# Performance work log

Hardware: AMD Instinct MI355X
Metric: run time of the kernel (lower is better)

## Reference

```python
import jax, jax.numpy as jnp
import numpy as np

GROUPS = 8   # GroupNorm groups used by create_pat_conv*_blocks(..., groups=8)
EPS = 1e-5
K = 20       # num_neighbor


def group_norm(x, gamma, beta):
    # x: [B, C, ...spatial]
    B, C = x.shape[0], x.shape[1]
    shape = x.shape
    xg = x.reshape(B, GROUPS, C // GROUPS, -1)
    m = xg.mean(axis=(2, 3), keepdims=True)
    v = ((xg - m) ** 2).mean(axis=(2, 3), keepdims=True)
    xg = (xg - m) * jax.lax.rsqrt(v + EPS)
    x = xg.reshape(shape)
    bshape = (1, C) + (1,) * (len(shape) - 2)
    return x * gamma.reshape(bshape) + beta.reshape(bshape)


def conv_block(x, w, b, gamma, beta):
    # pointwise (kernel-size 1) conv + GroupNorm + ELU, works for 1d and 2d spatial
    y = jnp.einsum('oc,bc...->bo...', w, x) + b.reshape((1, -1) + (1,) * (x.ndim - 2))
    return jax.nn.elu(group_norm(y, gamma, beta))


def knn_graph(points, k):
    # points: [B, 3, N] -> neighbor coords [B, 3, N, k] (self included, dilation=1)
    sq = jnp.sum(points * points, axis=1)                      # [B, N]
    inner = jnp.einsum('bci,bcj->bij', points, points)         # [B, N, N]
    dist = sq[:, :, None] + sq[:, None, :] - 2.0 * inner       # squared pairwise dist
    _, idx = jax.lax.top_k(-dist, k)                           # [B, N, k] smallest dists
    neighbors = jnp.take_along_axis(points[:, :, None, :], idx[:, None, :, :], axis=3)
    return neighbors                                           # [B, 3, N, k]


def setup_inputs() -> dict:
    key = jax.random.key(0)
    B, N = 4, 8192
    dims1 = [6, 32, 64]
    dims2 = [64, 512, 1024]
    keys = iter(jax.random.split(key, 32))
    inp = {"points": jax.random.normal(next(keys), (B, 3, N), dtype=jnp.float32)}
    for tag, dims in (("p1", dims1), ("p2", dims2)):
        for i in range(len(dims) - 1):
            cin, cout = dims[i], dims[i + 1]
            inp[f"{tag}_w{i}"] = jax.random.normal(next(keys), (cout, cin), dtype=jnp.float32) / np.float32(np.sqrt(cin))
            inp[f"{tag}_b{i}"] = jnp.zeros((cout,), dtype=jnp.float32)
            inp[f"{tag}_g{i}"] = jnp.ones((cout,), dtype=jnp.float32)
            inp[f"{tag}_beta{i}"] = jnp.zeros((cout,), dtype=jnp.float32)
    return inp


def reference(points, p1_w0, p1_b0, p1_g0, p1_beta0, p1_w1, p1_b1, p1_g1, p1_beta1,
              p2_w0, p2_b0, p2_g0, p2_beta0, p2_w1, p2_b1, p2_g1, p2_beta1):
    neighbors = knn_graph(points, K)                             # [B, 3, N, K]
    center = jnp.broadcast_to(points[:, :, :, None], neighbors.shape)
    x = jnp.concatenate([center, neighbors - center], axis=1)   # [B, 6, N, K]
    x = conv_block(x, p1_w0, p1_b0, p1_g0, p1_beta0)            # [B, 32, N, K]
    x = conv_block(x, p1_w1, p1_b1, p1_g1, p1_beta1)            # [B, 64, N, K]
    x = jnp.max(x, axis=2)                                      # [B, 64, K] (faithful to source: max over dim=2)
    x = conv_block(x, p2_w0, p2_b0, p2_g0, p2_beta0)            # [B, 512, K]
    x = conv_block(x, p2_w1, p2_b1, p2_g1, p2_beta1)            # [B, 1024, K]
    return x
```

## Files before the change

kernel.cpp:

```cpp
#include <hip/hip_runtime.h>
#include <math.h>

#define NPTS   8192
#define BATCH  4
#define KNN    20
#define NKTOT  (NPTS*KNN)
#define EPS    1e-5f
#define QC2    16
#define FQC    64

#define WINW   3072
#define WITR   (WINW/4/128)
#define NBIN   1024
#define BIN_LO (-4.5f)
#define BIN_W  (9.0f/1024.0f)

typedef float v2f __attribute__((ext_vector_type(2)));

__device__ __forceinline__ float elu(float x) { return x > 0.0f ? x : expm1f(x); }
__device__ __forceinline__ float eluf(float x) { return x > 0.0f ? x : __expf(x) - 1.0f; }
__device__ __forceinline__ v2f splat2(float x) { v2f v; v.x = x; v.y = x; return v; }
__device__ __forceinline__ float rfl(float x) {
    return __uint_as_float(__builtin_amdgcn_readfirstlane(__float_as_uint(x)));
}

__device__ __forceinline__ unsigned fenc(float f) {
    unsigned b = __float_as_uint(f);
    return b ^ ((unsigned)(((int)b) >> 31) | 0x80000000u);
}
__device__ __forceinline__ float fdec(unsigned u) {
    unsigned b = (u & 0x80000000u) ? (u ^ 0x80000000u) : ~u;
    return __uint_as_float(b);
}

__device__ __forceinline__ int xbin(float x) {
    int bin = (int)floorf((x + 4.5f) * (1024.0f / 9.0f));
    return bin < 0 ? 0 : (bin > NBIN - 1 ? NBIN - 1 : bin);
}

__device__ __forceinline__ unsigned long long packkey(float s, int orig, int slot) {
    return ((unsigned long long)fenc(s) << 32)
         | (unsigned)(((NPTS - 1 - orig) << 13) | slot);
}

__global__ __launch_bounds__(256) void prep_kernel(const float* __restrict__ points,
                                                   float4* __restrict__ pts4,
                                                   float* __restrict__ zeroreg,
                                                   unsigned* __restrict__ minenc,
                                                   unsigned* __restrict__ fcnt)
{
    const int t = blockIdx.x * 256 + threadIdx.x;
    const int b = t >> 13, n = t & (NPTS - 1);
    const float* px = points + b * 3 * NPTS;
    float x = px[n], y = px[NPTS + n], z = px[2 * NPTS + n];
    pts4[t] = make_float4(x, y, z, -0.5f * (x * x + y * y + z * z));
    if (t < 18176) zeroreg[t] = 0.f;
    if (t < 5120)  minenc[t] = 0xFFFFFFFFu;
    if (t < 4)     fcnt[t] = 0u;
}

__global__ __launch_bounds__(1024) void hist_kernel(const float* __restrict__ points,
                                                    int* __restrict__ Pcur)
{
    __shared__ int h[NBIN];
    __shared__ int sc[NBIN];
    const int b = blockIdx.x;
    const int t = threadIdx.x;
    h[t] = 0;
    __syncthreads();
    const float* px = points + b * 3 * NPTS;
    for (int i = t; i < NPTS; i += 1024)
        atomicAdd(&h[xbin(px[i])], 1);
    __syncthreads();
    int v = h[t];
    sc[t] = v;
    __syncthreads();
    for (int off = 1; off < NBIN; off <<= 1) {
        int a = (t >= off) ? sc[t - off] : 0;
        __syncthreads();
        sc[t] += a;
        __syncthreads();
    }
    Pcur[b * NBIN + t] = sc[t] - v;
}

__global__ __launch_bounds__(256) void scatter_kernel(const float4* __restrict__ pts4,
                                                      int* __restrict__ Pcur,
                                                      float4* __restrict__ psort,
                                                      int* __restrict__ sidx,
                                                      int* __restrict__ binof)
{
    const int t = blockIdx.x * 256 + threadIdx.x;
    const int b = t >> 13, n = t & (NPTS - 1);
    float4 p = pts4[t];
    int bin = xbin(p.x);
    int slot = atomicAdd(&Pcur[b * NBIN + bin], 1);
    psort[b * NPTS + slot] = p;
    sidx [b * NPTS + slot] = n;
    binof[b * NPTS + slot] = bin;
}

__global__ __launch_bounds__(256, 8) void knn_win_kernel(
    const float4* __restrict__ psort, const int* __restrict__ sidx,
    const int* __restrict__ binof, int* __restrict__ idx_out,
    unsigned* __restrict__ fcnt, int* __restrict__ flist)
{
    __shared__ unsigned long long queue[32][QC2];
    __shared__ float smaxs[4][8][64];
    __shared__ float gates[8];
    __shared__ int qcnt[32];

    const int tid  = threadIdx.x;
    const int lane = tid & 63;
    const int wv   = tid >> 6;
    const int b    = blockIdx.x >> 10;
    const int oct  = blockIdx.x & 1023;
    const int q0s  = oct * 8;
    const float4* psb = psort + b * NPTS;
    const int*    six = sidx  + b * NPTS;
    const int*    bob = binof + b * NPTS;

    int s = q0s + 4 - WINW / 2;
    if (s < 0) s = 0;
    if (s > NPTS - WINW) s = NPTS - WINW;

    if (tid < 32) qcnt[tid] = 0;

    float qx[8], qy[8], qz[8], q2[8];
    v2f smax2[8];
#pragma unroll
    for (int q = 0; q < 8; ++q) {
        float4 qp = psb[q0s + q];
        qx[q] = rfl(qp.x); qy[q] = rfl(qp.y); qz[q] = rfl(qp.z);
        q2[q] = rfl(-(qp.w + qp.w));
        smax2[q] = splat2(-INFINITY);
    }

    const int lbase = s + (((lane >> 5) * 4 + wv) << 6) + ((lane & 31) << 1);

#pragma unroll 3
    for (int t = 0; t < WITR; ++t) {
        float4 p0 = psb[lbase + t * 512];
        float4 p1 = psb[lbase + t * 512 + 1];
        v2f px = { p0.x, p1.x }, py = { p0.y, p1.y };
        v2f pz = { p0.z, p1.z }, pw = { p0.w, p1.w };
#pragma unroll
        for (int q = 0; q < 8; ++q) {
            v2f sv = __builtin_elementwise_fma(splat2(qx[q]), px,
                     __builtin_elementwise_fma(splat2(qy[q]), py,
                     __builtin_elementwise_fma(splat2(qz[q]), pz, pw)));
            smax2[q] = __builtin_elementwise_max(smax2[q], sv);
        }
    }
#pragma unroll
    for (int q = 0; q < 8; ++q) smaxs[wv][q][lane] = fmaxf(smax2[q].x, smax2[q].y);
    __syncthreads();

#pragma unroll
    for (int qq = 0; qq < 2; ++qq) {
        const int q = wv * 2 + qq;
        float v = fmaxf(fmaxf(smaxs[0][q][lane], smaxs[1][q][lane]),
                        fmaxf(smaxs[2][q][lane], smaxs[3][q][lane]));
#pragma unroll
        for (int k = 2; k <= 64; k <<= 1)
#pragma unroll
            for (int j = k >> 1; j >= 1; j >>= 1) {
                float o = __shfl_xor(v, j);
                bool up = ((lane & k) == 0);
                bool keepmin = (((lane & j) == 0) == up);
                v = keepmin ? fminf(v, o) : fmaxf(v, o);
            }
        float m = __shfl(v, 44);
        if (lane == 0) gates[q] = m - 1e-4f - 1e-5f * fabsf(m);
    }
    __syncthreads();
    float sgate[8];
#pragma unroll
    for (int q = 0; q < 8; ++q) sgate[q] = gates[q];

    for (int t = 0; t < WITR; ++t) {
        const int jb = lbase + t * 512;
        float4 p0 = psb[jb];
        float4 p1 = psb[jb + 1];
        v2f px = { p0.x, p1.x }, py = { p0.y, p1.y };
        v2f pz = { p0.z, p1.z }, pw = { p0.w, p1.w };
#pragma unroll
        for (int q = 0; q < 8; ++q) {
            v2f sv = __builtin_elementwise_fma(splat2(qx[q]), px,
                     __builtin_elementwise_fma(splat2(qy[q]), py,
                     __builtin_elementwise_fma(splat2(qz[q]), pz, pw)));
            if (fmaxf(sv.x, sv.y) >= sgate[q]) {
#pragma unroll
                for (int h = 0; h < 2; ++h) {
                    float svh = h ? sv.y : sv.x;
                    if (svh >= sgate[q]) {
                        int slot = atomicAdd(&qcnt[wv * 8 + q], 1);
                        if (slot < QC2)
                            queue[wv * 8 + q][slot] = packkey(svh, six[jb + h], jb + h);
                    }
                }
            }
        }
    }
    __syncthreads();

    float xLe = (s == 0) ? -3.0e38f
                         : (BIN_LO + (float)(bob[s] + 1) * BIN_W);
    float xRe = (s == NPTS - WINW) ? 3.0e38f
                         : (BIN_LO + (float)bob[s + WINW] * BIN_W);

#pragma unroll
    for (int qq = 0; qq < 2; ++qq) {
        const int q = wv * 2 + qq;
        int c0r = qcnt[0 * 8 + q], c1r = qcnt[1 * 8 + q];
        int c2r = qcnt[2 * 8 + q], c3r = qcnt[3 * 8 + q];
        const bool ovf = (c0r > QC2) || (c1r > QC2) || (c2r > QC2) || (c3r > QC2);
        int c0 = c0r < QC2 ? c0r : QC2;
        int c1 = c1r < QC2 ? c1r : QC2;
        int c2 = c2r < QC2 ? c2r : QC2;
        int c3 = c3r < QC2 ? c3r : QC2;
        int b1 = c0, b2 = c0 + c1, b3 = c0 + c1 + c2, b4 = b3 + c3;
        unsigned long long key = 0ull;
        if (lane < b1)      key = queue[0 * 8 + q][lane];
        else if (lane < b2) key = queue[1 * 8 + q][lane - b1];
        else if (lane < b3) key = queue[2 * 8 + q][lane - b2];
        else if (lane < b4) key = queue[3 * 8 + q][lane - b3];
#pragma unroll
        for (int k = 2; k <= 64; k <<= 1)
#pragma unroll
            for (int j = k >> 1; j >= 1; j >>= 1) {
                unsigned long long o = __shfl_xor(key, j);
                bool up = ((lane & k) == 0);
                bool keepmax = (((lane & j) == 0) == up);
                bool omax = o > key;
                key = (keepmax == omax) ? o : key;
            }
        if (lane < KNN)
            idx_out[(b * KNN + lane) * NPTS + (q0s + q)] =
                (int)(unsigned)(key & 0x1FFFu);

        unsigned long long k19 = __shfl(key, 19);
        float s20 = fdec((unsigned)(k19 >> 32));
        float d20 = fmaxf(q2[q] - 2.0f * s20, 0.0f);
        float mg  = 1e-3f + 1e-3f * d20;
        float dL  = qx[q] - xLe;
        float dR  = xRe - qx[q];
        bool ok = !ovf && dL > 0.0f && dR > 0.0f
                  && (d20 + mg < dL * dL) && (d20 + mg < dR * dR);
        if (!ok && lane == 0) {
            unsigned fs = atomicAdd(&fcnt[b], 1u);
            if (fs < 8192u) flist[b * 8192 + fs] = q0s + q;
        }
    }
}

__global__ __launch_bounds__(256, 8) void knn_fb_kernel(const float4* __restrict__ psort,
                                                        const int* __restrict__ sidx,
                                                        int* __restrict__ idx_out,
                                                        const unsigned* __restrict__ fcnt,
                                                        const int* __restrict__ flist)
{
    __shared__ unsigned long long queue[2][FQC];
    __shared__ float smaxs[4][2][64];
    __shared__ float gates[2];
    __shared__ int qcnt[2];

    const int tid  = threadIdx.x;
    const int lane = tid & 63;
    const int wv   = tid >> 6;
    const int bb   = blockIdx.x & 3;
    unsigned cnt = fcnt[bb];
    if (cnt > 8192u) cnt = 8192u;
    if (cnt == 0u) return;
    const float4* pb = psort + bb * NPTS;
    const int* six = sidx + bb * NPTS;
    const int* fl = flist + bb * 8192;
    const int cbase = wv * (NPTS / 4);
    const int tstep = gridDim.x >> 2;

    for (int task = blockIdx.x >> 2; task * 2 < (int)cnt; task += tstep) {
        int qs[2];
        float qx[2], qy[2], qz[2];
        v2f smax2[2];
        if (tid < 2) qcnt[tid] = 0;
#pragma unroll
        for (int q = 0; q < 2; ++q) {
            int e = task * 2 + q;
            if (e >= (int)cnt) e = (int)cnt - 1;
            qs[q] = __builtin_amdgcn_readfirstlane(fl[e]);
            float4 qp = pb[qs[q]];
            qx[q] = rfl(qp.x); qy[q] = rfl(qp.y); qz[q] = rfl(qp.z);
            smax2[q] = splat2(-INFINITY);
        }

#pragma unroll 4
        for (int t = 0; t < NPTS / 4 / 128; ++t) {
            float4 p0 = pb[cbase + t * 128 + 2 * lane];
            float4 p1 = pb[cbase + t * 128 + 2 * lane + 1];
            v2f px = { p0.x, p1.x }, py = { p0.y, p1.y };
            v2f pz = { p0.z, p1.z }, pw = { p0.w, p1.w };
#pragma unroll
            for (int q = 0; q < 2; ++q) {
                v2f sv = __builtin_elementwise_fma(splat2(qx[q]), px,
                         __builtin_elementwise_fma(splat2(qy[q]), py,
                         __builtin_elementwise_fma(splat2(qz[q]), pz, pw)));
                smax2[q] = __builtin_elementwise_max(smax2[q], sv);
            }
        }
#pragma unroll
        for (int q = 0; q < 2; ++q) smaxs[wv][q][lane] = fmaxf(smax2[q].x, smax2[q].y);
        __syncthreads();

        if (wv < 2) {
            const int q = wv;
            float v = fmaxf(fmaxf(smaxs[0][q][lane], smaxs[1][q][lane]),
                            fmaxf(smaxs[2][q][lane], smaxs[3][q][lane]));
#pragma unroll
            for (int k = 2; k <= 64; k <<= 1)
#pragma unroll
                for (int j = k >> 1; j >= 1; j >>= 1) {
                    float o = __shfl_xor(v, j);
                    bool up = ((lane & k) == 0);
                    bool keepmin = (((lane & j) == 0) == up);
                    v = keepmin ? fminf(v, o) : fmaxf(v, o);
                }
            float m = __shfl(v, 44);
            if (lane == 0) gates[q] = m - 1e-4f - 1e-5f * fabsf(m);
        }
        __syncthreads();
        float sg0 = gates[0], sg1 = gates[1];

        for (int t = 0; t < NPTS / 4 / 128; ++t) {
            const int jb = cbase + t * 128 + 2 * lane;
            float4 p0 = pb[jb];
            float4 p1 = pb[jb + 1];
            v2f px = { p0.x, p1.x }, py = { p0.y, p1.y };
            v2f pz = { p0.z, p1.z }, pw = { p0.w, p1.w };
#pragma unroll
            for (int q = 0; q < 2; ++q) {
                float sg = q ? sg1 : sg0;
                v2f sv = __builtin_elementwise_fma(splat2(qx[q]), px,
                         __builtin_elementwise_fma(splat2(qy[q]), py,
                         __builtin_elementwise_fma(splat2(qz[q]), pz, pw)));
                if (fmaxf(sv.x, sv.y) >= sg) {
#pragma unroll
                    for (int h = 0; h < 2; ++h) {
                        float svh = h ? sv.y : sv.x;
                        if (svh >= sg) {
                            int slot = atomicAdd(&qcnt[q], 1);
                            if (slot < FQC)
                                queue[q][slot] = packkey(svh, six[jb + h], jb + h);
                        }
                    }
                }
            }
        }
        __syncthreads();

        if (wv < 2) {
            const int q = wv;
            int c = qcnt[q]; c = c < FQC ? c : FQC;
            unsigned long long key = (lane < c) ? queue[q][lane] : 0ull;
#pragma unroll
            for (int k = 2; k <= 64; k <<= 1)
#pragma unroll
                for (int j = k >> 1; j >= 1; j >>= 1) {
                    unsigned long long o = __shfl_xor(key, j);
                    bool up = ((lane & k) == 0);
                    bool keepmax = (((lane & j) == 0) == up);
                    bool omax = o > key;
                    key = (keepmax == omax) ? o : key;
                }
            if (lane < KNN)
                idx_out[(bb * KNN + lane) * NPTS + qs[q]] =
                    (int)(unsigned)(key & 0x1FFFu);
        }
        __syncthreads();
    }
}

__global__ __launch_bounds__(256) void moments_x_kernel(const float4* __restrict__ psort,
                                                        const int* __restrict__ idx,
                                                        float* __restrict__ sums1p)
{
    const int b  = blockIdx.x / 80;
    const int r0 = (blockIdx.x - b * 80) * 2048;
    const float4* pb = psort + b * NPTS;
    const int* ib = idx + b * NKTOT;

    float v[27];
#pragma unroll
    for (int i = 0; i < 27; ++i) v[i] = 0.f;

    for (int e = 0; e < 8; ++e) {
        const int id = r0 + e * 256 + threadIdx.x;
        const int n = id & (NPTS - 1);
        const int j = ib[id];
        float4 c4 = pb[n];
        float4 e4 = pb[j];
        float x[6] = { c4.x, c4.y, c4.z, e4.x - c4.x, e4.y - c4.y, e4.z - c4.z };
        int p = 6;
#pragma unroll
        for (int d = 0; d < 6; ++d) {
            v[d] += x[d];
#pragma unroll
            for (int ee = d; ee < 6; ++ee) v[p++] += x[d] * x[ee];
        }
    }
#pragma unroll
    for (int i = 0; i < 27; ++i)
        for (int o = 32; o > 0; o >>= 1) v[i] += __shfl_xor(v[i], o);

    __shared__ float red[4][27];
    const int lane = threadIdx.x & 63, w = threadIdx.x >> 6;
    if (lane == 0)
#pragma unroll
        for (int i = 0; i < 27; ++i) red[w][i] = v[i];
    __syncthreads();
    if (threadIdx.x < 27) {
        float acc = red[0][threadIdx.x] + red[1][threadIdx.x] + red[2][threadIdx.x] + red[3][threadIdx.x];
        int slot = blockIdx.x & 63;
        atomicAdd(&sums1p[(slot * BATCH + b) * 27 + threadIdx.x], acc);
    }
}

__global__ void finalize1_kernel(const float* __restrict__ sums1p,
                                 const float* __restrict__ w1, const float* __restrict__ b1,
                                 const float* __restrict__ g1, const float* __restrict__ beta1,
                                 float* __restrict__ w1f)
{
    __shared__ float S[BATCH][27];
    const int t = threadIdx.x;
    if (t < 108) {
        int b = t / 27, i = t % 27;
        float acc = 0.f;
        for (int s = 0; s < 64; ++s) acc += sums1p[(s * BATCH + b) * 27 + i];
        S[b][i] = acc;
    }
    __syncthreads();
    const int b = t >> 5, c = t & 31;
    const float invS = 1.0f / (float)NKTOT;
    float Ex[6], M[6][6];
#pragma unroll
    for (int d = 0; d < 6; ++d) Ex[d] = S[b][d] * invS;
    int p = 6;
#pragma unroll
    for (int d = 0; d < 6; ++d)
#pragma unroll
        for (int e = d; e < 6; ++e) { float v = S[b][p++] * invS; M[d][e] = v; M[e][d] = v; }
    const int g = c >> 2;
    float msum = 0.f, qsum = 0.f;
    for (int cc = g * 4; cc < g * 4 + 4; ++cc) {
        float w[6];
#pragma unroll
        for (int d = 0; d < 6; ++d) w[d] = w1[cc * 6 + d];
        float dotEx = 0.f;
#pragma unroll
        for (int d = 0; d < 6; ++d) dotEx += w[d] * Ex[d];
        float Ey = dotEx + b1[cc];
        float Ey2 = 0.f;
#pragma unroll
        for (int d = 0; d < 6; ++d)
#pragma unroll
            for (int e = 0; e < 6; ++e) Ey2 += w[d] * w[e] * M[d][e];
        Ey2 += 2.0f * b1[cc] * dotEx + b1[cc] * b1[cc];
        msum += Ey; qsum += Ey2;
    }
    float m = msum * 0.25f;
    float var = qsum * 0.25f - m * m;
    float inv = rsqrtf(var + EPS);
    float s = g1[c] * inv;
    float tt = s * (b1[c] - m) + beta1[c];
    float* o = w1f + (b * 32 + c) * 8;
#pragma unroll
    for (int d = 0; d < 6; ++d) o[d] = s * w1[c * 6 + d];
    o[6] = tt; o[7] = 0.f;
}

__global__ __launch_bounds__(256, 3) void fused_main_kernel(
    const float4* __restrict__ psort, const int* __restrict__ idxb,
    const float* __restrict__ w1f, const float* __restrict__ w2, const float* __restrict__ b2,
    float* __restrict__ sums2p, unsigned int* __restrict__ maxenc, unsigned int* __restrict__ minenc)
{
    __shared__ __align__(16) float w2t[32 * 64];
    __shared__ __align__(16) float z1s[32 * 256];
    __shared__ __align__(16) float4 w1s4[64];
    __shared__ float b2s[64];
    __shared__ float redmx[256], redmn[256], sqred[64];

    const int t   = threadIdx.x;
    const int blk = blockIdx.x;
    const int nc  = blk & 15;
    const int k   = (blk >> 4) % 20;
    const int b   = blk / 320;

    for (int i = t; i < 512; i += 256) {
        float4 v = ((const float4*)w2)[i];
        int c = i >> 3, kq = (i & 7) * 4;
        w2t[(kq + 0) * 64 + c] = v.x; w2t[(kq + 1) * 64 + c] = v.y;
        w2t[(kq + 2) * 64 + c] = v.z; w2t[(kq + 3) * 64 + c] = v.w;
    }
    if (t < 64) { w1s4[t] = ((const float4*)w1f)[b * 64 + t]; b2s[t] = b2[t]; }

    const int wvi = t >> 6;
    const int cg8 = t & 7;
    const int n0  = (t >> 3) * 8;
    const int c0  = cg8 * 8;
    const float4* pb = psort + b * NPTS;
    const int nbase = nc * 512;
    const int* idxrow = idxb + (b * KNN + k) * NPTS;

    float mx[8], mn[8];
#pragma unroll
    for (int ci = 0; ci < 8; ++ci) { mx[ci] = -INFINITY; mn[ci] = INFINITY; }
    float gs = 0.f, gq = 0.f;

    for (int ph = 0; ph < 2; ++ph) {
        const int n = nbase + ph * 256 + t;
        const int j = idxrow[n];
        float4 c4 = pb[n];
        float4 e4 = pb[j];
        float x0[6] = { c4.x, c4.y, c4.z, e4.x - c4.x, e4.y - c4.y, e4.z - c4.z };

        __syncthreads();
#pragma unroll
        for (int c = 0; c < 32; ++c) {
            float4 wA = w1s4[c * 2 + 0];
            float4 wB = w1s4[c * 2 + 1];
            float z = wB.z;
            z = fmaf(wA.x, x0[0], z); z = fmaf(wA.y, x0[1], z); z = fmaf(wA.z, x0[2], z);
            z = fmaf(wA.w, x0[3], z); z = fmaf(wB.x, x0[4], z); z = fmaf(wB.y, x0[5], z);
            z1s[c * 256 + t] = eluf(z);
        }
        __syncthreads();

        float acc[8][8];
#pragma unroll
        for (int ci = 0; ci < 8; ++ci) {
            float bb = b2s[c0 + ci];
#pragma unroll
            for (int pj = 0; pj < 8; ++pj) acc[ci][pj] = bb;
        }
#pragma unroll
        for (int kk = 0; kk < 32; ++kk) {
            float4 a0 = *(const float4*)&w2t[kk * 64 + c0];
            float4 a1 = *(const float4*)&w2t[kk * 64 + c0 + 4];
            float4 z0 = *(const float4*)&z1s[kk * 256 + n0];
            float4 z1v = *(const float4*)&z1s[kk * 256 + n0 + 4];
            float avv[8] = { a0.x, a0.y, a0.z, a0.w, a1.x, a1.y, a1.z, a1.w };
            float zvv[8] = { z0.x, z0.y, z0.z, z0.w, z1v.x, z1v.y, z1v.z, z1v.w };
#pragma unroll
            for (int ci = 0; ci < 8; ++ci)
#pragma unroll
                for (int pj = 0; pj < 8; ++pj) acc[ci][pj] = fmaf(avv[ci], zvv[pj], acc[ci][pj]);
        }
#pragma unroll
        for (int ci = 0; ci < 8; ++ci)
#pragma unroll
            for (int pj = 0; pj < 8; ++pj) {
                float v = acc[ci][pj];
                gs += v; gq = fmaf(v, v, gq);
                mx[ci] = fmaxf(mx[ci], v); mn[ci] = fminf(mn[ci], v);
            }
    }

#pragma unroll
    for (int m = 8; m <= 32; m <<= 1) {
#pragma unroll
        for (int ci = 0; ci < 8; ++ci) {
            mx[ci] = fmaxf(mx[ci], __shfl_xor(mx[ci], m));
            mn[ci] = fminf(mn[ci], __shfl_xor(mn[ci], m));
        }
        gs += __shfl_xor(gs, m);
        gq += __shfl_xor(gq, m);
    }
    if ((t & 63) < 8) {
        const int l = t & 7;
#pragma unroll
        for (int ci = 0; ci < 8; ++ci) {
            redmx[wvi * 64 + l * 8 + ci] = mx[ci];
            redmn[wvi * 64 + l * 8 + ci] = mn[ci];
        }
        sqred[(wvi * 8 + l) * 2 + 0] = gs;
        sqred[(wvi * 8 + l) * 2 + 1] = gq;
    }
    __syncthreads();
    if (t < 64) {
        float m = fmaxf(fmaxf(redmx[t], redmx[64 + t]), fmaxf(redmx[128 + t], redmx[192 + t]));
        atomicMax(&maxenc[(b * 64 + t) * KNN + k], fenc(m));
    } else if (t < 128) {
        int c = t - 64;
        float m = fminf(fminf(redmn[c], redmn[64 + c]), fminf(redmn[128 + c], redmn[192 + c]));
        atomicMin(&minenc[(b * 64 + c) * KNN + k], fenc(m));
    } else if (t < 144) {
        int i2 = t - 128, g = i2 >> 1, w = i2 & 1;
        float v = 0.f;
#pragma unroll
        for (int wv2 = 0; wv2 < 4; ++wv2)
            v += sqred[(wv2 * 8 + g) * 2 + w];
        int slot = blk & 63;
        atomicAdd(&sums2p[((slot * BATCH + b) * 8 + g) * 2 + w], v);
    }
}

__global__ void build_m1_kernel(const float* __restrict__ sums2p,
                                const unsigned int* __restrict__ maxenc,
                                const unsigned int* __restrict__ minenc,
                                const float* __restrict__ gamma, const float* __restrict__ beta,
                                float* __restrict__ m1)
{
    const int t = blockIdx.x * 256 + threadIdx.x;
    const int b = t / 1280;
    const int r = t - b * 1280;
    const int c = r / 20;
    const int g = c >> 3;
    float s = 0.f, q = 0.f;
    for (int sl = 0; sl < 64; ++sl) {
        s += sums2p[((sl * BATCH + b) * 8 + g) * 2 + 0];
        q += sums2p[((sl * BATCH + b) * 8 + g) * 2 + 1];
    }
    const float cnt = 8.0f * (float)NKTOT;
    float m = s / cnt;
    float var = q / cnt - m * m;
    float inv = rsqrtf(var + EPS);
    float sc = gamma[c] * inv;
    float tt = beta[c] - sc * m;
    float y = (sc >= 0.f) ? fdec(maxenc[t]) : fdec(minenc[t]);
    m1[t] = elu(sc * y + tt);
}

template <int CIN, int SLOTS>
__global__ void p2_gemm_kernel(const float* __restrict__ zin, const float* __restrict__ w,
                               const float* __restrict__ bias, float* __restrict__ yout,
                               float* __restrict__ sumsp, int chans_per_group)
{
    const int t = blockIdx.x * 256 + threadIdx.x;
    const int per_b = (gridDim.x * 256) / BATCH;
    const int b = t / per_b;
    const int r = t - b * per_b;
    const int o = r / 20;
    const int k = r - o * 20;
    const float* zb = zin + b * CIN * 20;
    const float* wrow = w + o * CIN;
    float acc = bias[o];
    for (int c = 0; c < CIN; c += 4) {
        float4 wv = *(const float4*)&wrow[c];
        acc += wv.x * zb[(c + 0) * 20 + k] + wv.y * zb[(c + 1) * 20 + k]
             + wv.z * zb[(c + 2) * 20 + k] + wv.w * zb[(c + 3) * 20 + k];
    }
    yout[t] = acc;

    __shared__ float ls[16];
    if (threadIdx.x < 16) ls[threadIdx.x] = 0.f;
    __syncthreads();
    const int g = o / chans_per_group;
    atomicAdd(&ls[g * 2 + 0], acc);
    atomicAdd(&ls[g * 2 + 1], acc * acc);
    __syncthreads();
    if (threadIdx.x < 16) {
        int slot = blockIdx.x & (SLOTS - 1);
        atomicAdd(&sumsp[(slot * BATCH + b) * 16 + threadIdx.x], ls[threadIdx.x]);
    }
}

template <int SLOTS>
__global__ void p2_finalize_kernel(const float* __restrict__ y, const float* __restrict__ sumsp,
                                   const float* __restrict__ gamma, const float* __restrict__ beta,
                                   float* __restrict__ z, int chans_per_group, float cnt)
{
    const int t = blockIdx.x * 256 + threadIdx.x;
    const int per_b = (gridDim.x * 256) / BATCH;
    const int b = t / per_b;
    const int r = t - b * per_b;
    const int o = r / 20;
    const int g = o / chans_per_group;
    float s = 0.f, q = 0.f;
    for (int sl = 0; sl < SLOTS; ++sl) {
        s += sumsp[(sl * BATCH + b) * 16 + g * 2 + 0];
        q += sumsp[(sl * BATCH + b) * 16 + g * 2 + 1];
    }
    float m = s / cnt;
    float var = q / cnt - m * m;
    float inv = rsqrtf(var + EPS);
    float v = gamma[o] * inv * (y[t] - m) + beta[o];
    z[t] = elu(v);
}

extern "C" void kernel_launch(void* const* d_in, const int* in_sizes, int n_in,
                              void* d_out, int out_size, void* d_ws, size_t ws_size,
                              hipStream_t stream)
{
    const float* points  = (const float*)d_in[0];
    const float* p1_w0   = (const float*)d_in[1];
    const float* p1_b0   = (const float*)d_in[2];
    const float* p1_g0   = (const float*)d_in[3];
    const float* p1_bt0  = (const float*)d_in[4];
    const float* p1_w1   = (const float*)d_in[5];
    const float* p1_b1   = (const float*)d_in[6];
    const float* p1_g1   = (const float*)d_in[7];
    const float* p1_bt1  = (const float*)d_in[8];
    const float* p2_w0   = (const float*)d_in[9];
    const float* p2_b0   = (const float*)d_in[10];
    const float* p2_g0   = (const float*)d_in[11];
    const float* p2_bt0  = (const float*)d_in[12];
    const float* p2_w1   = (const float*)d_in[13];
    const float* p2_b1   = (const float*)d_in[14];
    const float* p2_g1   = (const float*)d_in[15];
    const float* p2_bt1  = (const float*)d_in[16];
    float* out = (float*)d_out;

    float* ws = (float*)d_ws;
    int*      idx     = (int*)ws;
    float*    sums1p  = ws + 655360;
    float*    sums2p  = sums1p + 6912;
    float*    sumsAp  = sums2p + 4096;
    float*    sumsBp  = sumsAp + 1024;
    unsigned* maxenc  = (unsigned*)(sumsBp + 1024);
    unsigned* minenc  = maxenc + 5120;
    float*    w1f     = (float*)(minenc + 5120);
    float*    m1      = w1f + 1024;
    float*    yp2a    = m1 + 5120;
    float*    zp2a    = yp2a + 40960;
    float*    yp2b    = zp2a + 40960;
    float4*   pts4    = (float4*)yp2a;
    float*    psortf  = yp2b + 81920;
    float4*   psort4  = (float4*)psortf;
    int*      sidx    = (int*)(psortf + 131072);
    int*      binof   = sidx + 32768;
    int*      Pcur    = binof + 32768 + 64;
    unsigned* fcnt4   = (unsigned*)(Pcur + 4096);
    int*      flist   = (int*)(fcnt4 + 64);

    prep_kernel<<<128, 256, 0, stream>>>(points, pts4, sums1p, minenc, fcnt4);
    hist_kernel<<<4, 1024, 0, stream>>>(points, Pcur);
    scatter_kernel<<<128, 256, 0, stream>>>(pts4, Pcur, psort4, sidx, binof);
    knn_win_kernel<<<4096, 256, 0, stream>>>(psort4, sidx, binof, idx, fcnt4, flist);
    knn_fb_kernel<<<4096, 256, 0, stream>>>(psort4, sidx, idx, fcnt4, flist);
    moments_x_kernel<<<320, 256, 0, stream>>>(psort4, idx, sums1p);
    finalize1_kernel<<<1, 128, 0, stream>>>(sums1p, p1_w0, p1_b0, p1_g0, p1_bt0, w1f);
    fused_main_kernel<<<1280, 256, 0, stream>>>(psort4, idx, w1f, p1_w1, p1_b1,
                                                sums2p, maxenc, minenc);
    build_m1_kernel<<<20, 256, 0, stream>>>(sums2p, maxenc, minenc, p1_g1, p1_bt1, m1);
    p2_gemm_kernel<64, 16><<<160, 256, 0, stream>>>(m1, p2_w0, p2_b0, yp2a, sumsAp, 64);
    p2_finalize_kernel<16><<<160, 256, 0, stream>>>(yp2a, sumsAp, p2_g0, p2_bt0, zp2a, 64, 1280.0f);
    p2_gemm_kernel<512, 16><<<320, 256, 0, stream>>>(zp2a, p2_w1, p2_b1, yp2b, sumsBp, 128);
    p2_finalize_kernel<16><<<320, 256, 0, stream>>>(yp2b, sumsBp, p2_g1, p2_bt1, out, 128, 2560.0f);
}
```

Baseline: 268.9 us.

## Shrink KNN gate window, merge per-wave queues, fold histogram into prep kernel

The KNN gating pass now estimates each query's 20th-best threshold from a narrower 2048-point window instead of the full 3072-point scan window, cutting the first-pass FMA work. The four per-wave candidate queues are merged into one shared 64-entry queue per query, which removes the multi-queue gather logic and adds a fallback when fewer than 20 candidates are collected. The histogram is now built per block inside the prep kernel and reduced in a scan kernel, replacing the 4-block histogram kernel. The narrower gate window gives a looser threshold, so more candidates pass, which adds more shared-memory atomics and may send more queries to the fallback kernel.

```diff
diff --git a/kernel.cpp b/kernel.cpp
--- a/kernel.cpp
+++ b/kernel.cpp
@@ -6,11 +6,12 @@
 #define KNN    20
 #define NKTOT  (NPTS*KNN)
 #define EPS    1e-5f
-#define QC2    16
 #define FQC    64
 
 #define WINW   3072
 #define WITR   (WINW/4/128)
+#define GWIN   2048
+#define GITR   (GWIN/4/128)
 #define NBIN   1024
 #define BIN_LO (-4.5f)
 #define BIN_W  (9.0f/1024.0f)
@@ -47,32 +48,36 @@
                                                    float4* __restrict__ pts4,
                                                    float* __restrict__ zeroreg,
                                                    unsigned* __restrict__ minenc,
-                                                   unsigned* __restrict__ fcnt)
-{
+                                                   unsigned* __restrict__ fcnt,
+                                                   int* __restrict__ Pcur_part)
+{
+    __shared__ int lh[NBIN];
     const int t = blockIdx.x * 256 + threadIdx.x;
     const int b = t >> 13, n = t & (NPTS - 1);
+    for (int i = threadIdx.x; i < NBIN; i += 256) lh[i] = 0;
     const float* px = points + b * 3 * NPTS;
     float x = px[n], y = px[NPTS + n], z = px[2 * NPTS + n];
     pts4[t] = make_float4(x, y, z, -0.5f * (x * x + y * y + z * z));
     if (t < 18176) zeroreg[t] = 0.f;
     if (t < 5120)  minenc[t] = 0xFFFFFFFFu;
     if (t < 4)     fcnt[t] = 0u;
-}
-
-__global__ __launch_bounds__(1024) void hist_kernel(const float* __restrict__ points,
+    __syncthreads();
+    atomicAdd(&lh[xbin(x)], 1);
+    __syncthreads();
+    for (int i = threadIdx.x; i < NBIN; i += 256)
+        Pcur_part[blockIdx.x * NBIN + i] = lh[i];
+}
+
+__global__ __launch_bounds__(1024) void scan_kernel(const int* __restrict__ Pcur_part,
                                                     int* __restrict__ Pcur)
 {
-    __shared__ int h[NBIN];
     __shared__ int sc[NBIN];
     const int b = blockIdx.x;
     const int t = threadIdx.x;
-    h[t] = 0;
-    __syncthreads();
-    const float* px = points + b * 3 * NPTS;
-    for (int i = t; i < NPTS; i += 1024)
-        atomicAdd(&h[xbin(px[i])], 1);
-    __syncthreads();
-    int v = h[t];
+    int v = 0;
+#pragma unroll 8
+    for (int p = 0; p < 32; ++p)
+        v += Pcur_part[(b * 32 + p) * NBIN + t];
     sc[t] = v;
     __syncthreads();
     for (int off = 1; off < NBIN; off <<= 1) {
@@ -105,10 +110,10 @@
     const int* __restrict__ binof, int* __restrict__ idx_out,
     unsigned* __restrict__ fcnt, int* __restrict__ flist)
 {
-    __shared__ unsigned long long queue[32][QC2];
+    __shared__ unsigned long long queue[8][FQC];
     __shared__ float smaxs[4][8][64];
     __shared__ float gates[8];
-    __shared__ int qcnt[32];
+    __shared__ int qcnt[8];
 
     const int tid  = threadIdx.x;
     const int lane = tid & 63;
@@ -123,8 +128,11 @@
     int s = q0s + 4 - WINW / 2;
     if (s < 0) s = 0;
     if (s > NPTS - WINW) s = NPTS - WINW;
-
-    if (tid < 32) qcnt[tid] = 0;
+    int gs = q0s + 4 - GWIN / 2;
+    if (gs < 0) gs = 0;
+    if (gs > NPTS - GWIN) gs = NPTS - GWIN;
+
+    if (tid < 8) qcnt[tid] = 0;
 
     float qx[8], qy[8], qz[8], q2[8];
     v2f smax2[8];
@@ -136,12 +144,13 @@
         smax2[q] = splat2(-INFINITY);
     }
 
-    const int lbase = s + (((lane >> 5) * 4 + wv) << 6) + ((lane & 31) << 1);
-
-#pragma unroll 3
-    for (int t = 0; t < WITR; ++t) {
-        float4 p0 = psb[lbase + t * 512];
-        float4 p1 = psb[lbase + t * 512 + 1];
+    const int gbase = gs + (((lane >> 5) * 4 + wv) << 6) + ((lane & 31) << 1);
+    const int lbase = s  + (((lane >> 5) * 4 + wv) << 6) + ((lane & 31) << 1);
+
+#pragma unroll
+    for (int t = 0; t < GITR; ++t) {
+        float4 p0 = psb[gbase + t * 512];
+        float4 p1 = psb[gbase + t * 512 + 1];
         v2f px = { p0.x, p1.x }, py = { p0.y, p1.y };
         v2f pz = { p0.z, p1.z }, pw = { p0.w, p1.w };
 #pragma unroll
@@ -178,6 +187,7 @@
 #pragma unroll
     for (int q = 0; q < 8; ++q) sgate[q] = gates[q];
 
+#pragma unroll
     for (int t = 0; t < WITR; ++t) {
         const int jb = lbase + t * 512;
         float4 p0 = psb[jb];
@@ -194,9 +204,9 @@
                 for (int h = 0; h < 2; ++h) {
                     float svh = h ? sv.y : sv.x;
                     if (svh >= sgate[q]) {
-                        int slot = atomicAdd(&qcnt[wv * 8 + q], 1);
-                        if (slot < QC2)
-                            queue[wv * 8 + q][slot] = packkey(svh, six[jb + h], jb + h);
+                        int slot = atomicAdd(&qcnt[q], 1);
+                        if (slot < FQC)
+                            queue[q][slot] = packkey(svh, six[jb + h], jb + h);
                     }
                 }
             }
@@ -212,19 +222,10 @@
 #pragma unroll
     for (int qq = 0; qq < 2; ++qq) {
         const int q = wv * 2 + qq;
-        int c0r = qcnt[0 * 8 + q], c1r = qcnt[1 * 8 + q];
-        int c2r = qcnt[2 * 8 + q], c3r = qcnt[3 * 8 + q];
-        const bool ovf = (c0r > QC2) || (c1r > QC2) || (c2r > QC2) || (c3r > QC2);
-        int c0 = c0r < QC2 ? c0r : QC2;
-        int c1 = c1r < QC2 ? c1r : QC2;
-        int c2 = c2r < QC2 ? c2r : QC2;
-        int c3 = c3r < QC2 ? c3r : QC2;
-        int b1 = c0, b2 = c0 + c1, b3 = c0 + c1 + c2, b4 = b3 + c3;
-        unsigned long long key = 0ull;
-        if (lane < b1)      key = queue[0 * 8 + q][lane];
-        else if (lane < b2) key = queue[1 * 8 + q][lane - b1];
-        else if (lane < b3) key = queue[2 * 8 + q][lane - b2];
-        else if (lane < b4) key = queue[3 * 8 + q][lane - b3];
+        const int cr = qcnt[q];
+        const bool ovf = (cr > FQC);
+        const int c = cr < FQC ? cr : FQC;
+        unsigned long long key = (lane < c) ? queue[q][lane] : 0ull;
 #pragma unroll
         for (int k = 2; k <= 64; k <<= 1)
 #pragma unroll
@@ -245,7 +246,7 @@
         float mg  = 1e-3f + 1e-3f * d20;
         float dL  = qx[q] - xLe;
         float dR  = xRe - qx[q];
-        bool ok = !ovf && dL > 0.0f && dR > 0.0f
+        bool ok = !ovf && (c >= KNN) && dL > 0.0f && dR > 0.0f
                   && (d20 + mg < dL * dL) && (d20 + mg < dR * dR);
         if (!ok && lane == 0) {
             unsigned fs = atomicAdd(&fcnt[b], 1u);
@@ -723,6 +724,7 @@
     float*    zp2a    = yp2a + 40960;
     float*    yp2b    = zp2a + 40960;
     float4*   pts4    = (float4*)yp2a;
+    int*      Pcur_part = idx;
     float*    psortf  = yp2b + 81920;
     float4*   psort4  = (float4*)psortf;
     int*      sidx    = (int*)(psortf + 131072);
@@ -731,8 +733,8 @@
     unsigned* fcnt4   = (unsigned*)(Pcur + 4096);
     int*      flist   = (int*)(fcnt4 + 64);
 
-    prep_kernel<<<128, 256, 0, stream>>>(points, pts4, sums1p, minenc, fcnt4);
-    hist_kernel<<<4, 1024, 0, stream>>>(points, Pcur);
+    prep_kernel<<<128, 256, 0, stream>>>(points, pts4, sums1p, minenc, fcnt4, Pcur_part);
+    scan_kernel<<<4, 1024, 0, stream>>>(Pcur_part, Pcur);
     scatter_kernel<<<128, 256, 0, stream>>>(pts4, Pcur, psort4, sidx, binof);
     knn_win_kernel<<<4096, 256, 0, stream>>>(psort4, sidx, binof, idx, fcnt4, flist);
     knn_fb_kernel<<<4096, 256, 0, stream>>>(psort4, sidx, idx, fcnt4, flist);
```

After: 268.9 us. Within noise of the previous version (-0.0%).
